# Performance work log

Hardware: AMD Instinct MI355X
Metric: run time of the kernel (lower is better)

## Reference

```python
import jax, jax.numpy as jnp
import numpy as np

B, T, C = 4, 2048, 1024
H, HS = 16, 64  # num_heads, head_size


def _rope_tables(seq_len, d):
    # RoFormer table: i = 1..d/2, theta_i = 1/10000^(2(i-1)/d)
    i = jnp.arange(1, d // 2 + 1, dtype=jnp.float32)
    thetas = 1.0 / (10000.0 ** (2.0 * (i - 1.0) / d))
    m_theta = jnp.arange(seq_len, dtype=jnp.float32)[:, None] * thetas  # [T, d/2]
    return jnp.sin(m_theta), jnp.cos(m_theta)


def _apply_rope(x, sin, cos):
    # x: [B, H, T, hs]; sin/cos: [T, hs/2] broadcast over B,H
    x1, x2 = x[..., 0::2], x[..., 1::2]
    return jnp.concatenate([x1 * cos - x2 * sin, x1 * sin + x2 * cos], axis=-1)


def setup_inputs() -> dict:
    key = jax.random.key(0)
    ks = jax.random.split(key, 5)
    s = 0.02
    return {
        "x": jax.random.normal(ks[0], (B, T, C), dtype=jnp.float32),
        "W_qkv": jax.random.normal(ks[1], (C, 3 * C), dtype=jnp.float32) * s,
        "b_qkv": jnp.zeros((3 * C,), dtype=jnp.float32),
        "W_o": jax.random.normal(ks[2], (C, C), dtype=jnp.float32) * s,
        "b_o": jnp.zeros((C,), dtype=jnp.float32),
    }


def reference(x, W_qkv, b_qkv, W_o, b_o):
    Bx, Tx, Cx = x.shape
    qkv = x @ W_qkv + b_qkv  # [B, T, 3C]
    q, k, v = jnp.split(qkv, 3, axis=-1)
    to_heads = lambda t: t.reshape(Bx, Tx, H, HS).transpose(0, 2, 1, 3)  # [B,H,T,hs]
    q, k, v = to_heads(q), to_heads(k), to_heads(v)

    sin, cos = _rope_tables(Tx, HS)
    q = _apply_rope(q, sin, cos)
    k = _apply_rope(k, sin, cos)

    scale = 1.0 / jnp.sqrt(jnp.asarray(HS, dtype=x.dtype))
    scores = jnp.einsum("bhqd,bhkd->bhqk", q, k) * scale
    causal = jnp.tril(jnp.ones((Tx, Tx), dtype=bool))
    scores = jnp.where(causal, scores, jnp.finfo(scores.dtype).min)
    attn = jax.nn.softmax(scores, axis=-1)
    out = jnp.einsum("bhqk,bhkd->bhqd", attn, v)  # [B,H,T,hs]
    out = out.transpose(0, 2, 1, 3).reshape(Bx, Tx, H * HS)
    return out @ W_o + b_o
```

## Files before the change

kernel.cpp:

```cpp
#include <hip/hip_runtime.h>
#include <math.h>

typedef float  f32x4 __attribute__((ext_vector_type(4)));
typedef float  f32x2 __attribute__((ext_vector_type(2)));
typedef __bf16 bf16x8 __attribute__((ext_vector_type(8)));
typedef unsigned short u16x8 __attribute__((ext_vector_type(8)));
typedef unsigned short u16x4 __attribute__((ext_vector_type(4)));

#define DEVI __device__ __forceinline__

constexpr int Bc = 4, Tc = 2048, Cc = 1024, Hc = 16, HSc = 64;
constexpr int Mc  = Bc * Tc;
constexpr int N1c = 3 * Cc;
constexpr int Kc  = Cc;

DEVI unsigned short f2bf(float f) {
    unsigned u = __builtin_bit_cast(unsigned, f);
    u += 0x7FFFu + ((u >> 16) & 1u);
    return (unsigned short)(u >> 16);
}
DEVI float bf2f(unsigned short s) {
    unsigned u = ((unsigned)s) << 16;
    return __builtin_bit_cast(float, u);
}

typedef const __attribute__((address_space(1))) void* gbl_vp;
typedef __attribute__((address_space(3))) void* lds_vp;
DEVI void gload16(const unsigned short* g, unsigned short* l) {
    __builtin_amdgcn_global_load_lds((gbl_vp)g, (lds_vp)l, 16, 0, 0);
}

__global__ void rope_tab_kernel(f32x2* __restrict__ tab)
{
    const int i = blockIdx.x * blockDim.x + threadIdx.x;
    const int t = i >> 5, d = i & 31;
    float theta = exp2f(-(float)d * 0.41524101186186f);
    float s, c;
    sincosf((float)t * theta, &s, &c);
    f32x2 v; v[0] = c; v[1] = s;
    tab[i] = v;
}

__global__ void cvt_kernel(const float* __restrict__ in,
                           unsigned short* __restrict__ out)
{
    const size_t i = ((size_t)blockIdx.x * blockDim.x + threadIdx.x) * 8;
    f32x4 a = *reinterpret_cast<const f32x4*>(in + i);
    f32x4 b = *reinterpret_cast<const f32x4*>(in + i + 4);
    u16x8 o;
    o[0] = f2bf(a[0]); o[1] = f2bf(a[1]); o[2] = f2bf(a[2]); o[3] = f2bf(a[3]);
    o[4] = f2bf(b[0]); o[5] = f2bf(b[1]); o[6] = f2bf(b[2]); o[7] = f2bf(b[3]);
    *reinterpret_cast<u16x8*>(out + i) = o;
}

__global__ void wt_kernel(const float* __restrict__ W,
                          unsigned short* __restrict__ Wt, int N, int K)
{
    __shared__ unsigned short Ts[64][72];
    const int tid = threadIdx.x;
    const int n0 = blockIdx.x * 64, k0 = blockIdx.y * 64;

    #pragma unroll
    for (int i = 0; i < 4; ++i) {
        int kr = (tid >> 4) + i * 16, nc = (tid & 15) * 4;
        f32x4 v = *reinterpret_cast<const f32x4*>(W + (size_t)(k0 + kr) * N + n0 + nc);
        #pragma unroll
        for (int e = 0; e < 4; ++e) Ts[kr][nc + e] = f2bf(v[e]);
    }
    __syncthreads();
    #pragma unroll
    for (int i = 0; i < 2; ++i) {
        int s = tid * 2 + i;
        int n = s >> 3, k8 = (s & 7) * 8;
        u16x8 o;
        #pragma unroll
        for (int j = 0; j < 8; ++j) o[j] = Ts[k8 + j][n];
        *reinterpret_cast<u16x8*>(Wt + (size_t)(n0 + n) * K + k0 + k8) = o;
    }
}

template <int MODE, int NCOLS>
__global__ void gemm_kernel(const unsigned short* __restrict__ A,
                            const unsigned short* __restrict__ Bt,
                            const float* __restrict__ bias,
                            const f32x2* __restrict__ rope_t,
                            unsigned short* __restrict__ q_out,
                            unsigned short* __restrict__ k_out,
                            unsigned short* __restrict__ v_out,
                            float* __restrict__ f_out)
{
    __shared__ unsigned short As[128 * 64];
    __shared__ unsigned short Bs[128 * 64];

    const int tid  = threadIdx.x;
    const int lane = tid & 63, wid = tid >> 6;
    const int wr = wid >> 1, wc = wid & 1;
    const int lrow = lane & 15, lk = lane >> 4;

    const int xcd = blockIdx.x & 7, loc = blockIdx.x >> 3;
    const int m0 = (xcd * 8 + (loc & 7)) * 128;
    const int n0 = (loc >> 3) * 128;

    f32x4 acc[4][4] = {};

    for (int kt = 0; kt < Kc / 64; ++kt) {
        const int k0 = kt * 64;
        #pragma unroll
        for (int i = 0; i < 4; ++i) {
            const int s   = ((i * 4 + wid) << 6) + lane;
            const int row = s >> 3;
            const int gc  = (s & 7) ^ (row & 7);
            gload16(A  + (size_t)(m0 + row) * Kc + k0 + gc * 8, &As[(i * 4 + wid) << 9]);
            gload16(Bt + (size_t)(n0 + row) * Kc + k0 + gc * 8, &Bs[(i * 4 + wid) << 9]);
        }
        __syncthreads();

        #pragma unroll
        for (int kk = 0; kk < 2; ++kk) {
            bf16x8 a[4], b[4];
            #pragma unroll
            for (int mt = 0; mt < 4; ++mt) {
                const int ra = wr * 64 + mt * 16 + lrow;
                a[mt] = __builtin_bit_cast(bf16x8,
                    *reinterpret_cast<const u16x8*>(&As[ra * 64 + (((kk * 4 + lk) ^ (ra & 7)) << 3)]));
            }
            #pragma unroll
            for (int nt = 0; nt < 4; ++nt) {
                const int rb = wc * 64 + nt * 16 + lrow;
                b[nt] = __builtin_bit_cast(bf16x8,
                    *reinterpret_cast<const u16x8*>(&Bs[rb * 64 + (((kk * 4 + lk) ^ (rb & 7)) << 3)]));
            }
            #pragma unroll
            for (int mt = 0; mt < 4; ++mt)
                #pragma unroll
                for (int nt = 0; nt < 4; ++nt)
                    acc[mt][nt] = __builtin_amdgcn_mfma_f32_16x16x32_bf16(a[mt], b[nt], acc[mt][nt], 0, 0, 0);
        }
        __syncthreads();
    }

    #pragma unroll
    for (int mt = 0; mt < 4; ++mt) {
        #pragma unroll
        for (int nt = 0; nt < 4; ++nt) {
            #pragma unroll
            for (int r = 0; r < 4; ++r) {
                int grow = m0 + wr * 64 + mt * 16 + lk * 4 + r;
                int gcol = n0 + wc * 64 + nt * 16 + lrow;
                float val = acc[mt][nt][r] + bias[gcol];
                if constexpr (MODE == 0) {
                    int tsel = gcol >> 10;
                    int cc   = gcol & 1023;
                    int h    = cc >> 6, hs = cc & 63;
                    int bb   = grow >> 11, t = grow & (Tc - 1);
                    int bh   = bb * Hc + h;
                    if (tsel == 2) {
                        v_out[((size_t)bh * HSc + hs) * Tc + t] = f2bf(val);
                    } else {
                        float partner = __shfl_xor(val, 1, 64);
                        const bool ev = !(lrow & 1);
                        float x1 = ev ? val : partner;
                        float x2 = ev ? partner : val;
                        int d = hs >> 1;
                        f32x2 cs = rope_t[t * 32 + d];
                        float o = ev ? (x1 * cs[0] - x2 * cs[1])
                                     : (x1 * cs[1] + x2 * cs[0]);
                        int hs_out = ev ? d : d + 32;
                        unsigned short* dst = (tsel == 0) ? q_out : k_out;
                        dst[((size_t)bh * Tc + t) * HSc + hs_out] = f2bf(o);
                    }
                } else {
                    f_out[(size_t)grow * Cc + gcol] = val;
                }
            }
        }
    }
}

__launch_bounds__(256, 3)
__global__ void attn_kernel(const unsigned short* __restrict__ Q,
                            const unsigned short* __restrict__ K,
                            const unsigned short* __restrict__ Vt,
                            unsigned short* __restrict__ O)
{
    constexpr int PST = 72;
    __shared__ unsigned short Ks[2][64 * 64];
    __shared__ unsigned short Vs[2][64 * 64];
    __shared__ unsigned short Pl[4 * 16 * PST];

    const int tid = threadIdx.x, lane = tid & 63, wid = tid >> 6;
    const int lrow = lane & 15, lk = lane >> 4;

    const int xcd = blockIdx.x & 7, loc = blockIdx.x >> 3;
    const int bh  = xcd * 8 + (loc & 7);
    const int qs  = 15 - (loc >> 3);
    const int b = bh >> 4, h = bh & 15;

    const unsigned short* Qb = Q  + (size_t)bh * Tc  * HSc;
    const unsigned short* Kb = K  + (size_t)bh * Tc  * HSc;
    const unsigned short* Vb = Vt + (size_t)bh * HSc * Tc;
    unsigned short* pl = &Pl[wid * 16 * PST];

    auto stage = [&](int buf, int kt) {
        const int kv0 = kt * 64;
        #pragma unroll
        for (int rr = 0; rr < 2; ++rr) {
            const int s   = ((rr * 4 + wid) << 6) + lane;
            const int row = s >> 3;
            const int gc  = (s & 7) ^ (row & 7);
            gload16(Kb + (size_t)(kv0 + row) * HSc + gc * 8, &Ks[buf][(rr * 4 + wid) << 9]);
            gload16(Vb + (size_t)row * Tc + kv0 + gc * 8,    &Vs[buf][(rr * 4 + wid) << 9]);
        }
    };

    constexpr float sc = 0.18033688011112042f;

    const int wq0 = qs * 128 + wid * 32;
    const int ntile = 2 * qs + 2;

    bf16x8 qf[2][2];
    #pragma unroll
    for (int f = 0; f < 2; ++f)
        #pragma unroll
        for (int ks = 0; ks < 2; ++ks)
            qf[f][ks] = __builtin_bit_cast(bf16x8,
                *reinterpret_cast<const u16x8*>(Qb + (size_t)(wq0 + f * 16 + lrow) * HSc + ks * 32 + lk * 8));

    f32x4 Oacc[2][4] = {};
    float lsum[2][4] = {};

    stage(0, 0);
    for (int kt = 0; kt < ntile; ++kt) {
        const int kv0 = kt * 64;
        const int cur = kt & 1;
        const bool pre = (kt + 1 < ntile);
        if (pre) stage(cur ^ 1, kt + 1);
        if (pre) asm volatile("s_waitcnt vmcnt(4)" ::: "memory");
        else     asm volatile("s_waitcnt vmcnt(0)" ::: "memory");
        __builtin_amdgcn_s_barrier();

        if (kv0 <= wq0 + 31) {
            f32x4 S[2][4] = {};
            #pragma unroll
            for (int ct = 0; ct < 4; ++ct) {
                const int ro = ct * 16 + lrow;
                bf16x8 kf[2];
                #pragma unroll
                for (int ks = 0; ks < 2; ++ks)
                    kf[ks] = __builtin_bit_cast(bf16x8,
                        *reinterpret_cast<const u16x8*>(&Ks[cur][ro * 64 + (((ks * 4 + lk) ^ (ro & 7)) << 3)]));
                #pragma unroll
                for (int f = 0; f < 2; ++f)
                    #pragma unroll
                    for (int ks = 0; ks < 2; ++ks)
                        S[f][ct] = __builtin_amdgcn_mfma_f32_16x16x32_bf16(qf[f][ks], kf[ks], S[f][ct], 0, 0, 0);
            }

            bf16x8 pf[2][2];
            #pragma unroll
            for (int f = 0; f < 2; ++f) {
                const bool mf = (kv0 + 63 > wq0 + f * 16);
                #pragma unroll
                for (int ct = 0; ct < 4; ++ct)
                    #pragma unroll
                    for (int r = 0; r < 4; ++r) {
                        float s = S[f][ct][r] * sc;
                        if (mf && (kv0 + ct * 16 + lrow > wq0 + f * 16 + lk * 4 + r)) s = -1e30f;
                        float pv = __builtin_amdgcn_exp2f(s);
                        lsum[f][r] += pv;
                        pl[(lk * 4 + r) * PST + ct * 16 + lrow] =
                            __builtin_bit_cast(unsigned short, (__bf16)pv);
                    }
                asm volatile("s_waitcnt lgkmcnt(0)" ::: "memory");
                __builtin_amdgcn_sched_barrier(0);
                #pragma unroll
                for (int ks = 0; ks < 2; ++ks)
                    pf[f][ks] = __builtin_bit_cast(bf16x8,
                        *reinterpret_cast<const u16x8*>(&pl[lrow * PST + ks * 32 + lk * 8]));
                asm volatile("s_waitcnt lgkmcnt(0)" ::: "memory");
                __builtin_amdgcn_sched_barrier(0);
            }

            #pragma unroll
            for (int nt = 0; nt < 4; ++nt) {
                const int ro = nt * 16 + lrow;
                bf16x8 vf[2];
                #pragma unroll
                for (int ks = 0; ks < 2; ++ks)
                    vf[ks] = __builtin_bit_cast(bf16x8,
                        *reinterpret_cast<const u16x8*>(&Vs[cur][ro * 64 + (((ks * 4 + lk) ^ (ro & 7)) << 3)]));
                #pragma unroll
                for (int f = 0; f < 2; ++f)
                    #pragma unroll
                    for (int ks = 0; ks < 2; ++ks)
                        Oacc[f][nt] = __builtin_amdgcn_mfma_f32_16x16x32_bf16(pf[f][ks], vf[ks], Oacc[f][nt], 0, 0, 0);
            }
        }
        asm volatile("s_waitcnt lgkmcnt(0)" ::: "memory");
        __builtin_amdgcn_sched_barrier(0);
        __builtin_amdgcn_s_barrier();
    }

    #pragma unroll
    for (int f = 0; f < 2; ++f) {
        #pragma unroll
        for (int mk = 1; mk < 16; mk <<= 1)
            #pragma unroll
            for (int r = 0; r < 4; ++r) lsum[f][r] += __shfl_xor(lsum[f][r], mk, 64);
        #pragma unroll
        for (int r = 0; r < 4; ++r) {
            float inv = 1.0f / lsum[f][r];
            int t = wq0 + f * 16 + lk * 4 + r;
            #pragma unroll
            for (int nt = 0; nt < 4; ++nt) {
                int col = h * 64 + nt * 16 + lrow;
                O[((size_t)b * Tc + t) * Cc + col] = f2bf(Oacc[f][nt][r] * inv);
            }
        }
    }
}

extern "C" void kernel_launch(void* const* d_in, const int* in_sizes, int n_in,
                              void* d_out, int out_size, void* d_ws, size_t ws_size,
                              hipStream_t stream)
{
    const float* x    = (const float*)d_in[0];
    const float* Wqkv = (const float*)d_in[1];
    const float* bqkv = (const float*)d_in[2];
    const float* Wo   = (const float*)d_in[3];
    const float* bo   = (const float*)d_in[4];
    float* out = (float*)d_out;

    char* ws = (char*)d_ws;
    size_t off = 0;
    auto alloc = [&](size_t bytes) {
        void* p = ws + off;
        off += (bytes + 255) & ~(size_t)255;
        return p;
    };
    const size_t elems = (size_t)Bc * Hc * Tc * HSc;
    unsigned short* Qb  = (unsigned short*)alloc(elems * 2);
    unsigned short* Kb  = (unsigned short*)alloc(elems * 2);
    unsigned short* Vt  = (unsigned short*)alloc(elems * 2);
    unsigned short* Oa  = (unsigned short*)alloc(elems * 2);
    unsigned short* Xb  = (unsigned short*)alloc((size_t)Mc * Kc * 2);
    unsigned short* Wq_t = (unsigned short*)alloc((size_t)N1c * Kc * 2);
    unsigned short* Wo_t = (unsigned short*)alloc((size_t)Cc * Kc * 2);
    f32x2* Rt = (f32x2*)alloc((size_t)Tc * 32 * 8);

    rope_tab_kernel<<<(Tc * 32) / 256, 256, 0, stream>>>(Rt);
    cvt_kernel<<<(Mc * Kc) / (256 * 8), 256, 0, stream>>>(x, Xb);
    wt_kernel<<<dim3(N1c / 64, Kc / 64), 256, 0, stream>>>(Wqkv, Wq_t, N1c, Kc);
    wt_kernel<<<dim3(Cc / 64, Kc / 64), 256, 0, stream>>>(Wo, Wo_t, Cc, Kc);

    gemm_kernel<0, N1c><<<(N1c / 128) * (Mc / 128), 256, 0, stream>>>(
        Xb, Wq_t, bqkv, Rt, Qb, Kb, Vt, nullptr);
    attn_kernel<<<1024, 256, 0, stream>>>(Qb, Kb, Vt, Oa);
    gemm_kernel<1, Cc><<<(Cc / 128) * (Mc / 128), 256, 0, stream>>>(
        Oa, Wo_t, bo, nullptr, nullptr, nullptr, nullptr, out);
}
```

Measured before the change: 198.4 us.

## Stage V epilogue through LDS for coalesced stores and batch P round-trip

In the QKV GEMM epilogue, blocks producing V now transpose their tile through shared memory and write 16-byte contiguous chunks to the transposed V buffer. Previously each element was a scattered 2-byte store with stride Tc. Blocks producing Q and K select their destination pointer once per block. In attention, the per-wave P scratch is doubled so both 16-row fragments are written before a single wait, removing one LDS sync round-trip per tile at the cost of more shared memory per block, which could affect occupancy.

Result: faster. 184.3 us (-7.1%).

```diff
diff --git a/kernel.cpp b/kernel.cpp
--- a/kernel.cpp
+++ b/kernel.cpp
@@ -89,8 +89,9 @@
                             unsigned short* __restrict__ v_out,
                             float* __restrict__ f_out)
 {
-    __shared__ unsigned short As[128 * 64];
-    __shared__ unsigned short Bs[128 * 64];
+    __shared__ unsigned short SM[2 * 128 * 64];
+    unsigned short* As = SM;
+    unsigned short* Bs = SM + 128 * 64;
 
     const int tid  = threadIdx.x;
     const int lane = tid & 63, wid = tid >> 6;
@@ -139,41 +140,74 @@
         __syncthreads();
     }
 
-    #pragma unroll
-    for (int mt = 0; mt < 4; ++mt) {
-        #pragma unroll
-        for (int nt = 0; nt < 4; ++nt) {
-            #pragma unroll
-            for (int r = 0; r < 4; ++r) {
-                int grow = m0 + wr * 64 + mt * 16 + lk * 4 + r;
-                int gcol = n0 + wc * 64 + nt * 16 + lrow;
-                float val = acc[mt][nt][r] + bias[gcol];
-                if constexpr (MODE == 0) {
-                    int tsel = gcol >> 10;
-                    int cc   = gcol & 1023;
+    if constexpr (MODE == 1) {
+        #pragma unroll
+        for (int mt = 0; mt < 4; ++mt)
+            #pragma unroll
+            for (int nt = 0; nt < 4; ++nt)
+                #pragma unroll
+                for (int r = 0; r < 4; ++r) {
+                    int grow = m0 + wr * 64 + mt * 16 + lk * 4 + r;
+                    int gcol = n0 + wc * 64 + nt * 16 + lrow;
+                    f_out[(size_t)grow * Cc + gcol] = acc[mt][nt][r] + bias[gcol];
+                }
+    } else if (n0 >= 2 * Cc) {
+        unsigned short* Tv = SM;
+        const int bb = m0 >> 11, t0 = m0 & (Tc - 1);
+        #pragma unroll
+        for (int p = 0; p < 2; ++p) {
+            if (wc == p) {
+                #pragma unroll
+                for (int mt = 0; mt < 4; ++mt)
+                    #pragma unroll
+                    for (int nt = 0; nt < 4; ++nt)
+                        #pragma unroll
+                        for (int r = 0; r < 4; ++r) {
+                            int hs_l = nt * 16 + lrow;
+                            int t_l  = wr * 64 + mt * 16 + lk * 4 + r;
+                            int gcol = n0 + wc * 64 + nt * 16 + lrow;
+                            Tv[hs_l * 136 + t_l] = f2bf(acc[mt][nt][r] + bias[gcol]);
+                        }
+            }
+            __syncthreads();
+            const int h  = ((n0 - 2 * Cc) >> 6) + p;
+            const int bh = bb * Hc + h;
+            #pragma unroll
+            for (int i = 0; i < 4; ++i) {
+                int ch = i * 256 + tid;
+                int hs = ch >> 4, tc = ch & 15;
+                u16x8 v = *reinterpret_cast<const u16x8*>(&Tv[hs * 136 + tc * 8]);
+                *reinterpret_cast<u16x8*>(
+                    &v_out[((size_t)bh * HSc + hs) * Tc + t0 + tc * 8]) = v;
+            }
+            __syncthreads();
+        }
+    } else {
+        unsigned short* dst = (n0 < Cc) ? q_out : k_out;
+        #pragma unroll
+        for (int mt = 0; mt < 4; ++mt)
+            #pragma unroll
+            for (int nt = 0; nt < 4; ++nt)
+                #pragma unroll
+                for (int r = 0; r < 4; ++r) {
+                    int grow = m0 + wr * 64 + mt * 16 + lk * 4 + r;
+                    int gcol = n0 + wc * 64 + nt * 16 + lrow;
+                    float val = acc[mt][nt][r] + bias[gcol];
+                    int cc   = gcol & (Cc - 1);
                     int h    = cc >> 6, hs = cc & 63;
                     int bb   = grow >> 11, t = grow & (Tc - 1);
                     int bh   = bb * Hc + h;
-                    if (tsel == 2) {
-                        v_out[((size_t)bh * HSc + hs) * Tc + t] = f2bf(val);
-                    } else {
-                        float partner = __shfl_xor(val, 1, 64);
-                        const bool ev = !(lrow & 1);
-                        float x1 = ev ? val : partner;
-                        float x2 = ev ? partner : val;
-                        int d = hs >> 1;
-                        f32x2 cs = rope_t[t * 32 + d];
-                        float o = ev ? (x1 * cs[0] - x2 * cs[1])
-                                     : (x1 * cs[1] + x2 * cs[0]);
-                        int hs_out = ev ? d : d + 32;
-                        unsigned short* dst = (tsel == 0) ? q_out : k_out;
-                        dst[((size_t)bh * Tc + t) * HSc + hs_out] = f2bf(o);
-                    }
-                } else {
-                    f_out[(size_t)grow * Cc + gcol] = val;
+                    float partner = __shfl_xor(val, 1, 64);
+                    const bool ev = !(lrow & 1);
+                    float x1 = ev ? val : partner;
+                    float x2 = ev ? partner : val;
+                    int d = hs >> 1;
+                    f32x2 cs = rope_t[t * 32 + d];
+                    float o = ev ? (x1 * cs[0] - x2 * cs[1])
+                                 : (x1 * cs[1] + x2 * cs[0]);
+                    int hs_out = ev ? d : d + 32;
+                    dst[((size_t)bh * Tc + t) * HSc + hs_out] = f2bf(o);
                 }
-            }
-        }
     }
 }
 
@@ -186,7 +220,7 @@
     constexpr int PST = 72;
     __shared__ unsigned short Ks[2][64 * 64];
     __shared__ unsigned short Vs[2][64 * 64];
-    __shared__ unsigned short Pl[4 * 16 * PST];
+    __shared__ unsigned short Pl[4 * 32 * PST];
 
     const int tid = threadIdx.x, lane = tid & 63, wid = tid >> 6;
     const int lrow = lane & 15, lk = lane >> 4;
@@ -199,7 +233,7 @@
     const unsigned short* Qb = Q  + (size_t)bh * Tc  * HSc;
     const unsigned short* Kb = K  + (size_t)bh * Tc  * HSc;
     const unsigned short* Vb = Vt + (size_t)bh * HSc * Tc;
-    unsigned short* pl = &Pl[wid * 16 * PST];
+    unsigned short* pl = &Pl[wid * 32 * PST];
 
     auto stage = [&](int buf, int kt) {
         const int kv0 = kt * 64;
@@ -256,7 +290,6 @@
                         S[f][ct] = __builtin_amdgcn_mfma_f32_16x16x32_bf16(qf[f][ks], kf[ks], S[f][ct], 0, 0, 0);
             }
 
-            bf16x8 pf[2][2];
             #pragma unroll
             for (int f = 0; f < 2; ++f) {
                 const bool mf = (kv0 + 63 > wq0 + f * 16);
@@ -268,18 +301,19 @@
                         if (mf && (kv0 + ct * 16 + lrow > wq0 + f * 16 + lk * 4 + r)) s = -1e30f;
                         float pv = __builtin_amdgcn_exp2f(s);
                         lsum[f][r] += pv;
-                        pl[(lk * 4 + r) * PST + ct * 16 + lrow] =
+                        pl[(f * 16 + lk * 4 + r) * PST + ct * 16 + lrow] =
                             __builtin_bit_cast(unsigned short, (__bf16)pv);
                     }
-                asm volatile("s_waitcnt lgkmcnt(0)" ::: "memory");
-                __builtin_amdgcn_sched_barrier(0);
+            }
+            asm volatile("s_waitcnt lgkmcnt(0)" ::: "memory");
+            __builtin_amdgcn_sched_barrier(0);
+            bf16x8 pf[2][2];
+            #pragma unroll
+            for (int f = 0; f < 2; ++f)
                 #pragma unroll
                 for (int ks = 0; ks < 2; ++ks)
                     pf[f][ks] = __builtin_bit_cast(bf16x8,
-                        *reinterpret_cast<const u16x8*>(&pl[lrow * PST + ks * 32 + lk * 8]));
-                asm volatile("s_waitcnt lgkmcnt(0)" ::: "memory");
-                __builtin_amdgcn_sched_barrier(0);
-            }
+                        *reinterpret_cast<const u16x8*>(&pl[(f * 16 + lrow) * PST + ks * 32 + lk * 8]));
 
             #pragma unroll
             for (int nt = 0; nt < 4; ++nt) {
```
